# Kernel optimization log

Hardware: AMD Instinct MI355X
Metric: run time of the kernel (lower is better)

## Reference

```python
import jax, jax.numpy as jnp
import numpy as np

EPS_NORM = 1e-12
EPS_POS = 1e-05
MARGIN = 0.5


def l2_norm(x):
    # matches torch: x / sqrt(sum(x^2, axis=1) + 1e-12)
    norm = jnp.sqrt(jnp.sum(x * x, axis=1) + EPS_NORM)
    return x / norm[:, None]


def setup_inputs() -> dict:
    key = jax.random.key(0)
    k1, k2, k3, k4 = jax.random.split(key, 4)
    n, d, n_classes = 8192, 1024, 1024
    inputs_col = jax.random.normal(k1, (n, d), dtype=jnp.float32)
    inputs_row = jax.random.normal(k2, (n, d), dtype=jnp.float32)
    targets_col = jax.random.randint(k3, (n,), 0, n_classes)
    target_row = jax.random.randint(k4, (n,), 0, n_classes)
    return {"inputs_col": inputs_col, "targets_col": targets_col,
            "inputs_row": inputs_row, "target_row": target_row}


def reference(inputs_col, targets_col, inputs_row, target_row):
    n = inputs_col.shape[0]
    # [n, n] cosine similarity matrix
    sim = l2_norm(inputs_col) @ l2_norm(inputs_row).T
    same = targets_col[:, None] == target_row[None, :]  # [n, n] bool
    pos_mask = same & (sim < 1.0 - EPS_POS)
    neg_mask = (~same) & (sim > MARGIN)
    pos_loss = jnp.sum(jnp.where(pos_mask, 1.0 - sim, 0.0), axis=1)  # [n]
    neg_loss = jnp.sum(jnp.where(neg_mask, sim, 0.0), axis=1)        # [n]
    has_pos = jnp.any(pos_mask, axis=1)  # rows without valid positives are skipped
    row_loss = jnp.where(has_pos, pos_loss + neg_loss, 0.0)
    return jnp.sum(row_loss) / n
```

## Files before the change

### kernel.cpp

```cpp
#include <hip/hip_runtime.h>


constexpr int N = 8192;
constexpr int D = 1024;
constexpr int NT = D / 64;

typedef short bf16x8 __attribute__((ext_vector_type(8)));
typedef float f32x4 __attribute__((ext_vector_type(4)));

static __device__ inline unsigned short f2bf(float f) {
  unsigned int u = __float_as_uint(f);
  unsigned int r = (u + 0x7fffu + ((u >> 16) & 1u)) >> 16;
  return (unsigned short)r;
}

__global__ __launch_bounds__(256) void normalize_kernel(
    const float* __restrict__ in_col, const float* __restrict__ in_row,
    unsigned short* __restrict__ out_col, unsigned short* __restrict__ out_row) {
  int r = blockIdx.x * 4 + (threadIdx.x >> 6);
  int lane = threadIdx.x & 63;
  const float* in =
      (r < N) ? in_col + (size_t)r * D : in_row + (size_t)(r - N) * D;
  unsigned short* out =
      (r < N) ? out_col + (size_t)r * D : out_row + (size_t)(r - N) * D;
  float4 v[4];
  float s = 0.f;
#pragma unroll
  for (int c = 0; c < 4; c++) {
    v[c] = ((const float4*)in)[lane + c * 64];
    s += v[c].x * v[c].x + v[c].y * v[c].y + v[c].z * v[c].z + v[c].w * v[c].w;
  }
#pragma unroll
  for (int off = 32; off >= 1; off >>= 1) s += __shfl_xor(s, off, 64);
  float inv = 1.0f / sqrtf(s + 1e-12f);
#pragma unroll
  for (int c = 0; c < 4; c++) {
    ushort4 o;
    o.x = f2bf(v[c].x * inv);
    o.y = f2bf(v[c].y * inv);
    o.z = f2bf(v[c].z * inv);
    o.w = f2bf(v[c].w * inv);
    ((ushort4*)out)[lane + c * 64] = o;
  }
}

__global__ __launch_bounds__(512, 2) void loss_kernel(
    const unsigned short* __restrict__ An, const unsigned short* __restrict__ Bn,
    const int* __restrict__ tc, const int* __restrict__ tr,
    float* __restrict__ lossG, int* __restrict__ hasG) {
  __shared__ unsigned short lds[65536];

  const int tid = threadIdx.x;
  const int lane = tid & 63;
  const int wid = tid >> 6;
  const int wr = wid >> 2;
  const int wc = wid & 3;

  const int bid = blockIdx.x;
  const int x = bid & 7, s = bid >> 3;
  const int iBase = (((s & 7) | ((s >> 5) << 3))) * 256;
  const int jBase = (x * 4 + ((s >> 3) & 3)) * 256;

  const int frow = lane & 15;
  const int fkb = (lane >> 4) * 16;
  const int rxor = (lane & 7) << 4;
  const int kx0 = (0 + fkb) ^ rxor;
  const int kx1 = (64 + fkb) ^ rxor;
  int rowA[4], rowB[2];
#pragma unroll
  for (int m2 = 0; m2 < 4; m2++) rowA[m2] = (wr * 64 + m2 * 16 + frow) * 128;
#pragma unroll
  for (int n2 = 0; n2 < 2; n2++) rowB[n2] = (wc * 32 + n2 * 16 + frow) * 128;

  const int rl0 = tid >> 3;
  const int kel = (tid & 7) * 8;
  const int kSw = kel ^ ((rl0 & 7) << 3);
  const int rA0 = iBase + rl0;
  const int rB0 = jBase + ((rl0 >> 5) * 64) + (rl0 & 31);

#define GLDS(g, l)                                                        \
  __builtin_amdgcn_global_load_lds(                                       \
      (const __attribute__((address_space(1))) void*)(g),                 \
      (__attribute__((address_space(3))) void*)(l), 16, 0, 0)

#define STAGE_A(h, tt, P)                                                     \
  do {                                                                        \
    const int _k = ((tt) & 15) * 64 + kSw;                                    \
    unsigned short* _d = lds + (((P) * 2 + (h)) * 8192) + wid * 512;          \
    GLDS(An + (size_t)(rA0 + (h) * 64) * D + _k, _d);                         \
    GLDS(An + (size_t)(rA0 + 128 + (h) * 64) * D + _k, _d + 4096);            \
  } while (0)
#define STAGE_B(h, tt, P)                                                     \
  do {                                                                        \
    const int _k = ((tt) & 15) * 64 + kSw;                                    \
    unsigned short* _d = lds + 32768 + (((P) * 2 + (h)) * 8192) + wid * 512;  \
    GLDS(Bn + (size_t)(rB0 + (h) * 32) * D + _k, _d);                         \
    GLDS(Bn + (size_t)(rB0 + 128 + (h) * 32) * D + _k, _d + 4096);            \
  } while (0)

  f32x4 acc[8][4];
#pragma unroll
  for (int mi = 0; mi < 8; mi++)
#pragma unroll
    for (int ni = 0; ni < 4; ni++) acc[mi][ni] = (f32x4){0.f, 0.f, 0.f, 0.f};

  bf16x8 af[4][2], bf[2][2];
  const char* ldsc = (const char*)lds;

  STAGE_A(0, 0, 0);
  STAGE_B(0, 0, 0);
  STAGE_B(1, 0, 0);
  STAGE_A(1, 0, 0);
  STAGE_A(1, 1, 1);
  asm volatile("s_waitcnt vmcnt(2)" ::: "memory");
  __builtin_amdgcn_s_barrier();
  asm volatile("" ::: "memory");

#define PH(MIH, NIH, LOADA, LOADB, DA, DB, STG, PRE)                            \
  do {                                                                          \
    if (LOADA) {                                                                \
      _Pragma("unroll") for (int m2 = 0; m2 < 4; m2++) {                        \
        af[m2][0] = *(const bf16x8*)(ldsc + (DA) + (MIH) * 16384 + rowA[m2] + kx0); \
        af[m2][1] = *(const bf16x8*)(ldsc + (DA) + (MIH) * 16384 + rowA[m2] + kx1); \
      }                                                                         \
    }                                                                           \
    if (LOADB) {                                                                \
      _Pragma("unroll") for (int n2 = 0; n2 < 2; n2++) {                        \
        bf[n2][0] = *(const bf16x8*)(ldsc + (DB) + (NIH) * 16384 + rowB[n2] + kx0); \
        bf[n2][1] = *(const bf16x8*)(ldsc + (DB) + (NIH) * 16384 + rowB[n2] + kx1); \
      }                                                                         \
    }                                                                           \
    STG;                                                                        \
    if ((PRE) == 1) asm volatile("s_waitcnt lgkmcnt(0)" ::: "memory");          \
    if ((PRE) == 2) asm volatile("s_waitcnt vmcnt(2)" ::: "memory");            \
    asm volatile("" ::: "memory");                                              \
    __builtin_amdgcn_s_barrier();                                               \
    asm volatile("" ::: "memory");                                              \
    __builtin_amdgcn_s_setprio(1);                                              \
    _Pragma("unroll") for (int kk = 0; kk < 2; kk++)                            \
        _Pragma("unroll") for (int m2 = 0; m2 < 4; m2++)                        \
            _Pragma("unroll") for (int n2 = 0; n2 < 2; n2++)                    \
                acc[(MIH) * 4 + m2][(NIH) * 2 + n2] =                           \
                    __builtin_amdgcn_mfma_f32_16x16x32_bf16(                    \
                        af[m2][kk], bf[n2][kk],                                 \
                        acc[(MIH) * 4 + m2][(NIH) * 2 + n2], 0, 0, 0);          \
    __builtin_amdgcn_s_setprio(0);                                              \
  } while (0)

#define TILE(T, P)                                                              \
  do {                                                                          \
    PH(0, 0, true, true, (P)*32768, 65536 + (P)*32768,                          \
       STAGE_A(0, (T) + 1, 1 - (P)), 0);                                        \
    PH(0, 1, false, true, (P)*32768, 65536 + (P)*32768,                         \
       STAGE_B(0, (T) + 1, 1 - (P)), 0);                                        \
    PH(1, 1, true, false, (P)*32768, 65536 + (P)*32768,                         \
       STAGE_B(1, (T) + 1, 1 - (P)), 1);                                        \
    PH(1, 0, false, true, (P)*32768, 65536 + (P)*32768,                         \
       STAGE_A(1, (T) + 2, (P)), 2);                                            \
  } while (0)

  for (int tp = 0; tp < NT / 2; ++tp) {
    const int t0 = 2 * tp;
    TILE(t0, 0);
    TILE(t0 + 1, 1);
  }
  asm volatile("s_waitcnt vmcnt(0)" ::: "memory");
#undef TILE
#undef PH
#undef STAGE_A
#undef STAGE_B
#undef GLDS

  int trj[4];
#pragma unroll
  for (int ni = 0; ni < 4; ni++) trj[ni] = tr[jBase + wc * 64 + ni * 16 + frow];

#pragma unroll
  for (int mi = 0; mi < 8; mi++) {
#pragma unroll
    for (int r = 0; r < 4; r++) {
      const int i = iBase + wr * 128 + mi * 16 + (lane >> 4) * 4 + r;
      const int tci = tc[i];
      float v = 0.f;
      bool hasp = false;
#pragma unroll
      for (int ni = 0; ni < 4; ni++) {
        float s2 = acc[mi][ni][r];
        if (tci == trj[ni]) {
          if (s2 < 1.0f - 1e-5f) { v += 1.0f - s2; hasp = true; }
        } else if (s2 > 0.5f) {
          v += s2;
        }
      }
#pragma unroll
      for (int off = 1; off < 16; off <<= 1) v += __shfl_xor(v, off, 16);
      unsigned long long m = __ballot(hasp);
      bool rowHas = ((m >> ((lane >> 4) * 16)) & 0xFFFFull) != 0;
      if ((lane & 15) == 0) {
        if (v != 0.f) atomicAdd(&lossG[i], v);
        if (rowHas) atomicOr(&hasG[i], 1);
      }
    }
  }
}

__global__ __launch_bounds__(256) void finalize_kernel(
    const float* __restrict__ lossG, const int* __restrict__ hasG,
    float* __restrict__ out) {
  int tid = threadIdx.x;
  float s = 0.f;
  for (int i = tid; i < N; i += 256)
    if (hasG[i]) s += lossG[i];
#pragma unroll
  for (int off = 32; off >= 1; off >>= 1) s += __shfl_xor(s, off, 64);
  __shared__ float w4[4];
  if ((tid & 63) == 0) w4[tid >> 6] = s;
  __syncthreads();
  if (tid == 0) out[0] = (w4[0] + w4[1] + w4[2] + w4[3]) / (float)N;
}

extern "C" void kernel_launch(void* const* d_in, const int* in_sizes, int n_in,
                              void* d_out, int out_size, void* d_ws, size_t ws_size,
                              hipStream_t stream) {
  const float* in_col = (const float*)d_in[0];
  const int* tcol = (const int*)d_in[1];
  const float* in_row = (const float*)d_in[2];
  const int* trow = (const int*)d_in[3];
  float* out = (float*)d_out;

  char* ws = (char*)d_ws;
  float* lossG = (float*)ws;
  int* hasG = (int*)(ws + (size_t)N * 4);
  unsigned short* colN = (unsigned short*)(ws + (size_t)N * 8);
  unsigned short* rowN = colN + (size_t)N * D;

  hipMemsetAsync(ws, 0, (size_t)N * 8, stream);
  normalize_kernel<<<(2 * N) / 4, 256, 0, stream>>>(in_col, in_row, colN, rowN);
  loss_kernel<<<1024, 512, 0, stream>>>(colN, rowN, tcol, trow, lossG, hasG);
  finalize_kernel<<<1, 256, 0, stream>>>(lossG, hasG, out);
}
```

Measured before the change: 289.4 us.

## Restructure GEMM main loop to hold all A fragments and stream B per column

Reorganizes the four-phase MFMA schedule. Each tile now loads all eight A fragments once, then iterates over the four B column groups, loading only one B fragment pair per phase. Global-to-LDS prefetch is reordered so A halves for tile T+2 are issued earlier and drained with vmcnt(6) once per tile instead of mixed lgkmcnt/vmcnt waits. The aim is fewer LDS reads per MFMA and deeper prefetch, at the cost of more VGPRs for A fragments and tighter LDS buffer reuse hazards.

Result: no change. 294.2 us (+1.7%).

```diff
diff --git a/kernel.cpp b/kernel.cpp
--- a/kernel.cpp
+++ b/kernel.cpp
@@ -97,6 +97,9 @@
     GLDS(Bn + (size_t)(rB0 + (h) * 32) * D + _k, _d);                         \
     GLDS(Bn + (size_t)(rB0 + 128 + (h) * 32) * D + _k, _d + 4096);            \
   } while (0)
+#define STAGE_A1B0(tt, P) \
+  do { STAGE_A(1, tt, P); STAGE_B(0, tt, P); } while (0)
+#define STAGE_NONE do {} while (0)
 
   f32x4 acc[8][4];
 #pragma unroll
@@ -104,59 +107,57 @@
 #pragma unroll
     for (int ni = 0; ni < 4; ni++) acc[mi][ni] = (f32x4){0.f, 0.f, 0.f, 0.f};
 
-  bf16x8 af[4][2], bf[2][2];
+  bf16x8 af[8][2], bf[2];
   const char* ldsc = (const char*)lds;
 
   STAGE_A(0, 0, 0);
+  STAGE_A(1, 0, 0);
   STAGE_B(0, 0, 0);
   STAGE_B(1, 0, 0);
-  STAGE_A(1, 0, 0);
+  STAGE_A(0, 1, 1);
   STAGE_A(1, 1, 1);
-  asm volatile("s_waitcnt vmcnt(2)" ::: "memory");
+  STAGE_B(0, 1, 1);
+  asm volatile("s_waitcnt vmcnt(6)" ::: "memory");
   __builtin_amdgcn_s_barrier();
   asm volatile("" ::: "memory");
 
-#define PH(MIH, NIH, LOADA, LOADB, DA, DB, STG, PRE)                            \
+#define PH(NI, LOADAF, DA, DB, STG, DRN)                                        \
   do {                                                                          \
-    if (LOADA) {                                                                \
-      _Pragma("unroll") for (int m2 = 0; m2 < 4; m2++) {                        \
-        af[m2][0] = *(const bf16x8*)(ldsc + (DA) + (MIH) * 16384 + rowA[m2] + kx0); \
-        af[m2][1] = *(const bf16x8*)(ldsc + (DA) + (MIH) * 16384 + rowA[m2] + kx1); \
-      }                                                                         \
-    }                                                                           \
-    if (LOADB) {                                                                \
-      _Pragma("unroll") for (int n2 = 0; n2 < 2; n2++) {                        \
-        bf[n2][0] = *(const bf16x8*)(ldsc + (DB) + (NIH) * 16384 + rowB[n2] + kx0); \
-        bf[n2][1] = *(const bf16x8*)(ldsc + (DB) + (NIH) * 16384 + rowB[n2] + kx1); \
+    bf[0] = *(const bf16x8*)(ldsc + (DB) + ((NI) >> 1) * 16384 +                \
+                             rowB[(NI) & 1] + kx0);                             \
+    bf[1] = *(const bf16x8*)(ldsc + (DB) + ((NI) >> 1) * 16384 +                \
+                             rowB[(NI) & 1] + kx1);                             \
+    if (LOADAF) {                                                               \
+      _Pragma("unroll") for (int mh = 0; mh < 2; mh++)                          \
+          _Pragma("unroll") for (int m2 = 0; m2 < 4; m2++) {                    \
+        af[mh * 4 + m2][0] =                                                    \
+            *(const bf16x8*)(ldsc + (DA) + mh * 16384 + rowA[m2] + kx0);        \
+        af[mh * 4 + m2][1] =                                                    \
+            *(const bf16x8*)(ldsc + (DA) + mh * 16384 + rowA[m2] + kx1);        \
       }                                                                         \
     }                                                                           \
     STG;                                                                        \
-    if ((PRE) == 1) asm volatile("s_waitcnt lgkmcnt(0)" ::: "memory");          \
-    if ((PRE) == 2) asm volatile("s_waitcnt vmcnt(2)" ::: "memory");            \
+    if (DRN) asm volatile("s_waitcnt vmcnt(6)" ::: "memory");                   \
     asm volatile("" ::: "memory");                                              \
     __builtin_amdgcn_s_barrier();                                               \
     asm volatile("" ::: "memory");                                              \
     __builtin_amdgcn_s_setprio(1);                                              \
     _Pragma("unroll") for (int kk = 0; kk < 2; kk++)                            \
-        _Pragma("unroll") for (int m2 = 0; m2 < 4; m2++)                        \
-            _Pragma("unroll") for (int n2 = 0; n2 < 2; n2++)                    \
-                acc[(MIH) * 4 + m2][(NIH) * 2 + n2] =                           \
-                    __builtin_amdgcn_mfma_f32_16x16x32_bf16(                    \
-                        af[m2][kk], bf[n2][kk],                                 \
-                        acc[(MIH) * 4 + m2][(NIH) * 2 + n2], 0, 0, 0);          \
+        _Pragma("unroll") for (int m = 0; m < 8; m++)                           \
+            acc[m][NI] = __builtin_amdgcn_mfma_f32_16x16x32_bf16(               \
+                af[m][kk], bf[kk], acc[m][NI], 0, 0, 0);                        \
     __builtin_amdgcn_s_setprio(0);                                              \
   } while (0)
 
 #define TILE(T, P)                                                              \
   do {                                                                          \
-    PH(0, 0, true, true, (P)*32768, 65536 + (P)*32768,                          \
-       STAGE_A(0, (T) + 1, 1 - (P)), 0);                                        \
-    PH(0, 1, false, true, (P)*32768, 65536 + (P)*32768,                         \
-       STAGE_B(0, (T) + 1, 1 - (P)), 0);                                        \
-    PH(1, 1, true, false, (P)*32768, 65536 + (P)*32768,                         \
-       STAGE_B(1, (T) + 1, 1 - (P)), 1);                                        \
-    PH(1, 0, false, true, (P)*32768, 65536 + (P)*32768,                         \
-       STAGE_A(1, (T) + 2, (P)), 2);                                            \
+    PH(0, true, (P) * 32768, 65536 + (P) * 32768,                               \
+       STAGE_B(1, (T) + 1, 1 - (P)), 0);                                        \
+    PH(1, false, (P) * 32768, 65536 + (P) * 32768,                              \
+       STAGE_A(0, (T) + 2, (P)), 0);                                            \
+    PH(2, false, (P) * 32768, 65536 + (P) * 32768,                              \
+       STAGE_A1B0((T) + 2, (P)), 0);                                            \
+    PH(3, false, (P) * 32768, 65536 + (P) * 32768, STAGE_NONE, 1);              \
   } while (0)
 
   for (int tp = 0; tp < NT / 2; ++tp) {
@@ -167,6 +168,8 @@
   asm volatile("s_waitcnt vmcnt(0)" ::: "memory");
 #undef TILE
 #undef PH
+#undef STAGE_A1B0
+#undef STAGE_NONE
 #undef STAGE_A
 #undef STAGE_B
 #undef GLDS
```
